# Kernel tuning notes

Hardware: AMD Instinct MI355X
Metric: run time of the kernel (lower is better)

The kernel has to match this reference:

```python
import jax, jax.numpy as jnp
import numpy as np

B, V, H, NI, E = 512, 50, 768, 8, 2


def setup_inputs() -> dict:
    key = jax.random.key(0)
    ks = jax.random.split(key, 8)
    s1 = 1.0 / np.sqrt(2 * H)
    s = 1.0 / np.sqrt(H)
    return {
        "variable_states": jax.random.normal(ks[0], (B, V, H), jnp.float32),
        "edge_probs": jax.random.uniform(ks[1], (B, V, V, E), jnp.float32),
        "intervention_values": jax.random.normal(ks[2], (B, NI, H), jnp.float32),
        "W1": jax.random.normal(ks[3], (2 * H, H), jnp.float32) * s1,
        "b1": jnp.zeros((H,), jnp.float32),
        "W2": jax.random.normal(ks[4], (H, H), jnp.float32) * s,
        "b2": jnp.zeros((H,), jnp.float32),
        "Wg1": jax.random.normal(ks[5], (H, H), jnp.float32) * s,
        "bg1": jnp.zeros((H,), jnp.float32),
        "Wg2": jax.random.normal(ks[6], (H, 1), jnp.float32) * s,
        "bg2": jnp.zeros((1,), jnp.float32),
        "intervention_indices": jax.random.randint(ks[7], (B, NI), 0, V, jnp.int64),
    }


def _do_operator(variable_states, intervention_values, intervention_indices,
                 W1, b1, W2, b2, Wg1, bg1, Wg2, bg2):
    idx = intervention_indices                              # [B, NI]
    valid = (idx >= 0) & (idx < V)                          # [B, NI]
    idx_c = jnp.clip(idx, 0, V - 1)
    # gather all original vars for every intervention at once: [B, NI, H]
    orig = jnp.take_along_axis(variable_states, idx_c[..., None], axis=1)
    x = jnp.concatenate([orig, intervention_values], axis=-1)      # [B, NI, 2H]
    enc = jax.nn.gelu(x @ W1 + b1, approximate=False) @ W2 + b2    # [B, NI, H]
    gate = jax.nn.sigmoid(
        jax.nn.gelu(enc @ Wg1 + bg1, approximate=False) @ Wg2 + bg2
    )                                                              # [B, NI, 1]
    blended = orig * (1.0 - gate) + intervention_values * gate     # [B, NI, H]
    states = variable_states
    b_ar = jnp.arange(B)
    for i in range(NI):
        cur = states[b_ar, idx_c[:, i]]                            # [B, H]
        new = jnp.where(valid[:, i, None], blended[:, i], cur)
        states = states.at[b_ar, idx_c[:, i]].set(new)
    return states


def reference(variable_states, edge_probs, intervention_values,
              W1, b1, W2, b2, Wg1, bg1, Wg2, bg2, intervention_indices):
    # edge_probs is mutated in-place in the torch original but not returned;
    # the returned value is only the intervened states.
    return _do_operator(variable_states, intervention_values, intervention_indices,
                        W1, b1, W2, b2, Wg1, bg1, Wg2, bg2)
```

## Files before the change

### kernel.cpp

```cpp
#include <hip/hip_runtime.h>
#include <math.h>

#define B_  512
#define V_  50
#define H_  768
#define NI_ 8
#define M_  (B_ * NI_)
#define K1_ (2 * H_)
#define NCB_ 12

using f32x4 = __attribute__((ext_vector_type(4))) float;
using s16x8 = __attribute__((ext_vector_type(8))) short;

__device__ __forceinline__ float gelu_exact(float x) {
    return 0.5f * x * (1.0f + erff(x * 0.7071067811865476f));
}

__device__ __forceinline__ short f2bf(float f) {
    union { float f; unsigned u; } v; v.f = f;
    unsigned r = (v.u + 0x7fffu + ((v.u >> 16) & 1u)) >> 16;
    return (short)r;
}

#define GLOAD16(g, l)                                                          \
    __builtin_amdgcn_global_load_lds(                                          \
        (const __attribute__((address_space(1))) void*)(g),                    \
        (__attribute__((address_space(3))) void*)(l), 16, 0, 0)

__global__ __launch_bounds__(256) void pre_kernel(
    const float* __restrict__ vs, const float* __restrict__ iv,
    const int* __restrict__ idx,
    const float* __restrict__ W1, const float* __restrict__ W2,
    const float* __restrict__ Wg1,
    short* __restrict__ W1t, short* __restrict__ W2t, short* __restrict__ Wg1t,
    short* __restrict__ X, int* __restrict__ winner) {
    __shared__ short s[64][65];
    const int blk = blockIdx.x;
    const int tid = threadIdx.x;

    if (blk < 576) {
        const float* src; short* dst; int K, t;
        if (blk < 288)      { src = W1;  dst = W1t;  K = K1_; t = blk; }
        else if (blk < 432) { src = W2;  dst = W2t;  K = H_;  t = blk - 288; }
        else                { src = Wg1; dst = Wg1t; K = H_;  t = blk - 432; }
        int bx = t % 12, by = t / 12;
        int k0 = by * 64, n0 = bx * 64;
#pragma unroll
        for (int e = 0; e < 16; ++e) {
            int li = tid + e * 256;
            int kk = li >> 6, nn = li & 63;
            s[kk][nn] = f2bf(src[(size_t)(k0 + kk) * H_ + n0 + nn]);
        }
        __syncthreads();
#pragma unroll
        for (int e = 0; e < 16; ++e) {
            int li = tid + e * 256;
            int nn = li >> 6, kk = li & 63;
            dst[(size_t)(n0 + nn) * K + k0 + kk] = s[kk][nn];
        }
    } else if (blk < 1600) {
        int g = blk - 576;
        int r = g * 4 + (tid >> 6);
        int lane = tid & 63;
        int b = r >> 3;
        int id = idx[r];
        id = min(max(id, 0), V_ - 1);
        const float4* s1 = (const float4*)(vs + ((size_t)b * V_ + id) * H_);
        const float4* s2 = (const float4*)(iv + (size_t)r * H_);
        short* xr = X + (size_t)r * K1_;
#pragma unroll
        for (int part = 0; part < 3; ++part) {
            int e = lane + part * 64;
            float4 a = s1[e];
            float4 c = s2[e];
            short4 oa, oc;
            oa.x = f2bf(a.x); oa.y = f2bf(a.y); oa.z = f2bf(a.z); oa.w = f2bf(a.w);
            oc.x = f2bf(c.x); oc.y = f2bf(c.y); oc.z = f2bf(c.z); oc.w = f2bf(c.w);
            *(short4*)&xr[e * 4] = oa;
            *(short4*)&xr[H_ + e * 4] = oc;
        }
    } else {
        int b = (blk - 1600) * 256 + tid;
        if (b < B_) {
            int id[NI_];
#pragma unroll
            for (int i = 0; i < NI_; ++i) id[i] = idx[b * NI_ + i];
            for (int v = 0; v < V_; ++v) {
                int wv = -1;
#pragma unroll
                for (int i = 0; i < NI_; ++i)
                    if (id[i] == v) wv = i;
                winner[b * V_ + v] = wv;
            }
        }
    }
}

__device__ __forceinline__ short* lds_ptr(short* base, int row, int byteoff) {
    return (short*)((char*)base + row * 128 + (byteoff ^ ((row & 7) << 4)));
}

template <int ACT, int GATE>
__global__ __launch_bounds__(256) void gemm_mfma(
    const short* __restrict__ A,
    const short* __restrict__ Bt,
    const float* __restrict__ bias,
    short* __restrict__ C,
    int M, int N, int K,
    const float* __restrict__ wg2, float* __restrict__ gate_part) {
    __shared__ short As[2][128 * 64];
    __shared__ short Bs[2][64 * 64];

    const int tid = threadIdx.x;
    const int lane = tid & 63;
    const int wave = tid >> 6;
    const int llo = lane & 15;
    const int lhi = lane >> 4;

    int f = blockIdx.y * gridDim.x + blockIdx.x;
    int sw = (f & 7) * 48 + (f >> 3);
    int bx = sw % 12, by = sw / 12;
    const int row0 = by * 128;
    const int col0 = bx * 64;

    const short* gsrc[6];
    short* ldst0[6];
    int lstep[6];
#pragma unroll
    for (int p = 0; p < 6; ++p) {
        int c = wave * 6 + p;
        int jj = lane & 7;
        if (c < 16) {
            int r = c * 8 + (lane >> 3);
            int j = jj ^ (r & 7);
            gsrc[p] = A + (size_t)(row0 + r) * K + j * 8;
            ldst0[p] = &As[0][c * 512];
            lstep[p] = 128 * 64;
        } else {
            int r = (c - 16) * 8 + (lane >> 3);
            int j = jj ^ (r & 7);
            gsrc[p] = Bt + (size_t)(col0 + r) * K + j * 8;
            ldst0[p] = &Bs[0][(c - 16) * 512];
            lstep[p] = 64 * 64;
        }
    }

    f32x4 acc[2][4];
#pragma unroll
    for (int mi = 0; mi < 2; ++mi)
#pragma unroll
        for (int nf = 0; nf < 4; ++nf) acc[mi][nf] = (f32x4){0, 0, 0, 0};

    const int nt = K >> 6;
#pragma unroll
    for (int p = 0; p < 6; ++p) GLOAD16(gsrc[p], ldst0[p]);
    __syncthreads();

    for (int t = 0; t < nt; ++t) {
        const int cur = t & 1;
        if (t + 1 < nt) {
#pragma unroll
            for (int p = 0; p < 6; ++p)
                GLOAD16(gsrc[p] + (size_t)(t + 1) * 64,
                        ldst0[p] + (cur ^ 1) * lstep[p]);
        }
        short* Ab = (short*)As[cur];
        short* Bb = (short*)Bs[cur];
#pragma unroll
        for (int ks = 0; ks < 2; ++ks) {
            s16x8 a[2], b[4];
#pragma unroll
            for (int mi = 0; mi < 2; ++mi)
                a[mi] = *(const s16x8*)lds_ptr(Ab, wave * 32 + mi * 16 + llo,
                                               ks * 64 + lhi * 16);
#pragma unroll
            for (int nf = 0; nf < 4; ++nf)
                b[nf] = *(const s16x8*)lds_ptr(Bb, nf * 16 + llo,
                                               ks * 64 + lhi * 16);
#pragma unroll
            for (int mi = 0; mi < 2; ++mi)
#pragma unroll
                for (int nf = 0; nf < 4; ++nf)
                    acc[mi][nf] = __builtin_amdgcn_mfma_f32_16x16x32_bf16(
                        a[mi], b[nf], acc[mi][nf], 0, 0, 0);
        }
        __syncthreads();
    }

    if (!GATE) {
#pragma unroll
        for (int nf = 0; nf < 4; ++nf) {
            int cc = col0 + nf * 16 + llo;
            float bv = bias[cc];
#pragma unroll
            for (int mi = 0; mi < 2; ++mi) {
#pragma unroll
                for (int j = 0; j < 4; ++j) {
                    int rr = row0 + wave * 32 + mi * 16 + lhi * 4 + j;
                    float v = acc[mi][nf][j] + bv;
                    if (ACT) v = gelu_exact(v);
                    C[(size_t)rr * N + cc] = f2bf(v);
                }
            }
        }
    } else {
        float s[2][4];
#pragma unroll
        for (int mi = 0; mi < 2; ++mi)
#pragma unroll
            for (int j = 0; j < 4; ++j) s[mi][j] = 0.f;
#pragma unroll
        for (int nf = 0; nf < 4; ++nf) {
            int cc = col0 + nf * 16 + llo;
            float bv = bias[cc];
            float wv = wg2[cc];
#pragma unroll
            for (int mi = 0; mi < 2; ++mi)
#pragma unroll
                for (int j = 0; j < 4; ++j)
                    s[mi][j] += gelu_exact(acc[mi][nf][j] + bv) * wv;
        }
#pragma unroll
        for (int off = 1; off < 16; off <<= 1)
#pragma unroll
            for (int mi = 0; mi < 2; ++mi)
#pragma unroll
                for (int j = 0; j < 4; ++j)
                    s[mi][j] += __shfl_xor(s[mi][j], off);
        if (llo == 0) {
#pragma unroll
            for (int mi = 0; mi < 2; ++mi)
#pragma unroll
                for (int j = 0; j < 4; ++j) {
                    int rr = row0 + wave * 32 + mi * 16 + lhi * 4 + j;
                    gate_part[(size_t)rr * NCB_ + bx] = s[mi][j];
                }
        }
    }
}

__global__ __launch_bounds__(192) void final_write(
    const float* __restrict__ vs, const float* __restrict__ iv,
    const int* __restrict__ winner, const float* __restrict__ gate_part,
    const float* __restrict__ bg2, float* __restrict__ out) {
    int row = blockIdx.x;
    int t = threadIdx.x;
    const float4* src = (const float4*)(vs + (size_t)row * H_);
    float4* dst = (float4*)(out + (size_t)row * H_);
    int w = winner[row];
    if (w < 0) {
        dst[t] = src[t];
        return;
    }
    int b = row / V_;
    int r = b * NI_ + w;
    __shared__ float gsh;
    if (t == 0) {
        float s = bg2[0];
#pragma unroll
        for (int c = 0; c < NCB_; ++c) s += gate_part[(size_t)r * NCB_ + c];
        gsh = 1.f / (1.f + expf(-s));
    }
    __syncthreads();
    float g = gsh;
    const float4* ivr = (const float4*)(iv + (size_t)r * H_);
    float4 o = src[t], x = ivr[t], res;
    res.x = o.x * (1.f - g) + x.x * g;
    res.y = o.y * (1.f - g) + x.y * g;
    res.z = o.z * (1.f - g) + x.z * g;
    res.w = o.w * (1.f - g) + x.w * g;
    dst[t] = res;
}

extern "C" void kernel_launch(void* const* d_in, const int* in_sizes, int n_in,
                              void* d_out, int out_size, void* d_ws, size_t ws_size,
                              hipStream_t stream) {
    const float* vs  = (const float*)d_in[0];
    const float* iv  = (const float*)d_in[2];
    const float* W1  = (const float*)d_in[3];
    const float* b1  = (const float*)d_in[4];
    const float* W2  = (const float*)d_in[5];
    const float* b2  = (const float*)d_in[6];
    const float* Wg1 = (const float*)d_in[7];
    const float* bg1 = (const float*)d_in[8];
    const float* Wg2 = (const float*)d_in[9];
    const float* bg2 = (const float*)d_in[10];
    const int*   idx = (const int*)d_in[11];
    float* out = (float*)d_out;

    char* ws = (char*)d_ws;
    short* Xb   = (short*)ws;
    short* encb = Xb;
    short* h1b  = (short*)(ws + (size_t)M_ * K1_ * 2);
    float* gate_part = (float*)(ws + (size_t)M_ * K1_ * 2 + (size_t)M_ * H_ * 2);
    int*   winner = (int*)((char*)gate_part + (size_t)M_ * NCB_ * 4);
    short* W1t  = (short*)((char*)winner + (size_t)B_ * V_ * 4);
    short* W2t  = W1t + (size_t)H_ * K1_;
    short* Wg1t = W2t + (size_t)H_ * H_;

    pre_kernel<<<1602, 256, 0, stream>>>(vs, iv, idx, W1, W2, Wg1,
                                         W1t, W2t, Wg1t, Xb, winner);

    dim3 grid(H_ / 64, M_ / 128);
    gemm_mfma<1, 0><<<grid, 256, 0, stream>>>(Xb, W1t, b1, h1b, M_, H_, K1_, nullptr, nullptr);
    gemm_mfma<0, 0><<<grid, 256, 0, stream>>>(h1b, W2t, b2, encb, M_, H_, H_, nullptr, nullptr);
    gemm_mfma<1, 1><<<grid, 256, 0, stream>>>(encb, Wg1t, bg1, nullptr, M_, H_, H_, Wg2, gate_part);
    final_write<<<B_ * V_, 192, 0, stream>>>(vs, iv, winner, gate_part, bg2, out);
}
```

Before: 90.89 us.

## Overlap bulk state copy with GEMMs and blend only intervened rows

The bulk copy of variable_states into the output is split into three chunks, each handled by extra blocks appended to one of the three GEMM launches, so the copy runs alongside compute. The winner table is dropped. The final kernel now launches one block per intervention, skips it if a later intervention hits the same index (last write wins), and writes only the blended rows. This removes a full-tensor final pass and the winner precompute, but it adds idle copy blocks to each GEMM grid and relies on stream order so the blend writes land after the copies.

```diff
diff --git a/kernel.cpp b/kernel.cpp
--- a/kernel.cpp
+++ b/kernel.cpp
@@ -8,6 +8,9 @@
 #define M_  (B_ * NI_)
 #define K1_ (2 * H_)
 #define NCB_ 12
+#define NGEMM_ 384
+#define NCOPY_ 256
+#define COPY_PER_BLK_ 6400
 
 using f32x4 = __attribute__((ext_vector_type(4))) float;
 using s16x8 = __attribute__((ext_vector_type(8))) short;
@@ -33,7 +36,7 @@
     const float* __restrict__ W1, const float* __restrict__ W2,
     const float* __restrict__ Wg1,
     short* __restrict__ W1t, short* __restrict__ W2t, short* __restrict__ Wg1t,
-    short* __restrict__ X, int* __restrict__ winner) {
+    short* __restrict__ X) {
     __shared__ short s[64][65];
     const int blk = blockIdx.x;
     const int tid = threadIdx.x;
@@ -58,7 +61,7 @@
             int nn = li >> 6, kk = li & 63;
             dst[(size_t)(n0 + nn) * K + k0 + kk] = s[kk][nn];
         }
-    } else if (blk < 1600) {
+    } else {
         int g = blk - 576;
         int r = g * 4 + (tid >> 6);
         int lane = tid & 63;
@@ -79,20 +82,6 @@
             *(short4*)&xr[e * 4] = oa;
             *(short4*)&xr[H_ + e * 4] = oc;
         }
-    } else {
-        int b = (blk - 1600) * 256 + tid;
-        if (b < B_) {
-            int id[NI_];
-#pragma unroll
-            for (int i = 0; i < NI_; ++i) id[i] = idx[b * NI_ + i];
-            for (int v = 0; v < V_; ++v) {
-                int wv = -1;
-#pragma unroll
-                for (int i = 0; i < NI_; ++i)
-                    if (id[i] == v) wv = i;
-                winner[b * V_ + v] = wv;
-            }
-        }
     }
 }
 
@@ -107,18 +96,31 @@
     const float* __restrict__ bias,
     short* __restrict__ C,
     int M, int N, int K,
-    const float* __restrict__ wg2, float* __restrict__ gate_part) {
+    const float* __restrict__ wg2, float* __restrict__ gate_part,
+    const float4* __restrict__ cpy_src, float4* __restrict__ cpy_dst,
+    size_t cpy_base) {
     __shared__ short As[2][128 * 64];
     __shared__ short Bs[2][64 * 64];
 
     const int tid = threadIdx.x;
+    const int bid = blockIdx.x;
+
+    if (bid >= NGEMM_) {
+        size_t base = cpy_base + (size_t)(bid - NGEMM_) * COPY_PER_BLK_;
+#pragma unroll 5
+        for (int e = 0; e < COPY_PER_BLK_ / 256; ++e) {
+            size_t i = base + (size_t)e * 256 + tid;
+            cpy_dst[i] = cpy_src[i];
+        }
+        return;
+    }
+
     const int lane = tid & 63;
     const int wave = tid >> 6;
     const int llo = lane & 15;
     const int lhi = lane >> 4;
 
-    int f = blockIdx.y * gridDim.x + blockIdx.x;
-    int sw = (f & 7) * 48 + (f >> 3);
+    int sw = (bid & 7) * 48 + (bid >> 3);
     int bx = sw % 12, by = sw / 12;
     const int row0 = by * 128;
     const int col0 = bx * 64;
@@ -239,23 +241,18 @@
     }
 }
 
-__global__ __launch_bounds__(192) void final_write(
+__global__ __launch_bounds__(192) void final_blend(
     const float* __restrict__ vs, const float* __restrict__ iv,
-    const int* __restrict__ winner, const float* __restrict__ gate_part,
+    const int* __restrict__ idx, const float* __restrict__ gate_part,
     const float* __restrict__ bg2, float* __restrict__ out) {
-    int row = blockIdx.x;
-    int t = threadIdx.x;
-    const float4* src = (const float4*)(vs + (size_t)row * H_);
-    float4* dst = (float4*)(out + (size_t)row * H_);
-    int w = winner[row];
-    if (w < 0) {
-        dst[t] = src[t];
-        return;
-    }
-    int b = row / V_;
-    int r = b * NI_ + w;
+    int r = blockIdx.x;
+    int b = r >> 3, i = r & 7;
+    int id = idx[r];
+    if (id < 0 || id >= V_) return;
+    for (int j = i + 1; j < NI_; ++j)
+        if (idx[b * NI_ + j] == id) return;
     __shared__ float gsh;
-    if (t == 0) {
+    if (threadIdx.x == 0) {
         float s = bg2[0];
 #pragma unroll
         for (int c = 0; c < NCB_; ++c) s += gate_part[(size_t)r * NCB_ + c];
@@ -263,7 +260,10 @@
     }
     __syncthreads();
     float g = gsh;
+    int t = threadIdx.x;
+    const float4* src = (const float4*)(vs + ((size_t)b * V_ + id) * H_);
     const float4* ivr = (const float4*)(iv + (size_t)r * H_);
+    float4* dst = (float4*)(out + ((size_t)b * V_ + id) * H_);
     float4 o = src[t], x = ivr[t], res;
     res.x = o.x * (1.f - g) + x.x * g;
     res.y = o.y * (1.f - g) + x.y * g;
@@ -293,17 +293,23 @@
     short* encb = Xb;
     short* h1b  = (short*)(ws + (size_t)M_ * K1_ * 2);
     float* gate_part = (float*)(ws + (size_t)M_ * K1_ * 2 + (size_t)M_ * H_ * 2);
-    int*   winner = (int*)((char*)gate_part + (size_t)M_ * NCB_ * 4);
-    short* W1t  = (short*)((char*)winner + (size_t)B_ * V_ * 4);
+    short* W1t  = (short*)((char*)gate_part + (size_t)M_ * NCB_ * 4);
     short* W2t  = W1t + (size_t)H_ * K1_;
     short* Wg1t = W2t + (size_t)H_ * H_;
 
-    pre_kernel<<<1602, 256, 0, stream>>>(vs, iv, idx, W1, W2, Wg1,
-                                         W1t, W2t, Wg1t, Xb, winner);
-
-    dim3 grid(H_ / 64, M_ / 128);
-    gemm_mfma<1, 0><<<grid, 256, 0, stream>>>(Xb, W1t, b1, h1b, M_, H_, K1_, nullptr, nullptr);
-    gemm_mfma<0, 0><<<grid, 256, 0, stream>>>(h1b, W2t, b2, encb, M_, H_, H_, nullptr, nullptr);
-    gemm_mfma<1, 1><<<grid, 256, 0, stream>>>(encb, Wg1t, bg1, nullptr, M_, H_, H_, Wg2, gate_part);
-    final_write<<<B_ * V_, 192, 0, stream>>>(vs, iv, winner, gate_part, bg2, out);
-}
+    const float4* cs = (const float4*)vs;
+    float4* cd = (float4*)out;
+    const size_t CHUNK = (size_t)NCOPY_ * COPY_PER_BLK_;
+
+    pre_kernel<<<1600, 256, 0, stream>>>(vs, iv, idx, W1, W2, Wg1,
+                                         W1t, W2t, Wg1t, Xb);
+
+    const int nblk = NGEMM_ + NCOPY_;
+    gemm_mfma<1, 0><<<nblk, 256, 0, stream>>>(Xb, W1t, b1, h1b, M_, H_, K1_,
+                                              nullptr, nullptr, cs, cd, 0);
+    gemm_mfma<0, 0><<<nblk, 256, 0, stream>>>(h1b, W2t, b2, encb, M_, H_, H_,
+                                              nullptr, nullptr, cs, cd, CHUNK);
+    gemm_mfma<1, 1><<<nblk, 256, 0, stream>>>(encb, Wg1t, bg1, nullptr, M_, H_, H_,
+                                              Wg2, gate_part, cs, cd, 2 * CHUNK);
+    final_blend<<<M_, 192, 0, stream>>>(vs, iv, idx, gate_part, bg2, out);
+}
```

Result: faster. 81.36 us (-10.5%).
